# Kernel tuning notes

Hardware: AMD Instinct MI355X
Metric: run time of the kernel (lower is better)

## Reference

```python
import jax, jax.numpy as jnp
import numpy as np

EMBED_DIM = 1024
ATTN_DIM = 1024


def setup_inputs() -> dict:
    key = jax.random.key(0)
    k1, k2, k3, k4 = jax.random.split(key, 4)
    scale = 1.0 / np.sqrt(EMBED_DIM)
    return {
        "embedded": jax.random.normal(k1, (4, 2048, EMBED_DIM), dtype=jnp.float32),
        # weights stored as [in, out] (torch Linear applies x @ W.T)
        "Wk": jax.random.uniform(k2, (EMBED_DIM, ATTN_DIM), dtype=jnp.float32, minval=-scale, maxval=scale),
        "Wq": jax.random.uniform(k3, (EMBED_DIM, ATTN_DIM), dtype=jnp.float32, minval=-scale, maxval=scale),
        "Wv": jax.random.uniform(k4, (EMBED_DIM, ATTN_DIM), dtype=jnp.float32, minval=-scale, maxval=scale),
    }


def reference(embedded, Wk, Wq, Wv):
    b, t, _ = embedded.shape
    k = embedded @ Wk  # [b, t, d]
    q = embedded @ Wq
    v = embedded @ Wv
    scores = jnp.einsum("btd,bsd->bts", q, k) / jnp.sqrt(jnp.float32(k.shape[-1]))
    causal = jnp.tril(jnp.ones((t, t), dtype=bool))  # [t, t]
    scores = jnp.where(causal, scores, -jnp.inf)
    w = jax.nn.softmax(scores, axis=-1)
    o = jnp.einsum("bts,bsd->btd", w, v)
    return jnp.round(o * 10000.0) / 10000.0
```

## Files before the change

kernel.cpp:

```cpp
#include <hip/hip_runtime.h>
#include <cmath>

typedef _Float16 half8 __attribute__((ext_vector_type(8)));
typedef _Float16 half4 __attribute__((ext_vector_type(4)));
typedef float floatx4 __attribute__((ext_vector_type(4)));

__device__ __forceinline__ void load_lds16(const void* g, void* l) {
  __builtin_amdgcn_global_load_lds((const __attribute__((address_space(1))) void*)g,
                                   (__attribute__((address_space(3))) void*)l, 16, 0, 0);
}

__device__ __forceinline__ unsigned lds_addr(const void* p) {
  return (unsigned)(unsigned long long)(const __attribute__((address_space(3))) void*)p;
}

__device__ __forceinline__ half8 ds_read128(unsigned addr) {
  half8 r;
  asm volatile("ds_read_b128 %0, %1" : "=v"(r) : "v"(addr));
  return r;
}


__global__ void prep_kernel(const float* __restrict__ emb, const float* __restrict__ Wq,
                            const float* __restrict__ Wk, const float* __restrict__ Wv,
                            _Float16* __restrict__ Xp, _Float16* __restrict__ Wqp,
                            _Float16* __restrict__ Wkp, _Float16* __restrict__ Wvtp) {
  int p = blockIdx.x;
  if (p < 640) {
    __shared__ _Float16 lds[16 * 1032];
    const float* src;
    _Float16* dst;
    if (p < 512)      { src = emb + (size_t)p * 16384;        dst = Xp  + (size_t)p * 16384; }
    else if (p < 576) { src = Wq + (size_t)(p - 512) * 16384; dst = Wqp + (size_t)(p - 512) * 16384; }
    else              { src = Wk + (size_t)(p - 576) * 16384; dst = Wkp + (size_t)(p - 576) * 16384; }
    for (int it = 0; it < 16; ++it) {
      int idx = it * 256 + threadIdx.x;
      int row = idx >> 8, c4 = idx & 255;
      float4 v = ((const float4*)src)[row * 256 + c4];
      half4 h;
      h[0] = (_Float16)v.x; h[1] = (_Float16)v.y; h[2] = (_Float16)v.z; h[3] = (_Float16)v.w;
      *(half4*)(lds + row * 1032 + c4 * 4) = h;
    }
    __syncthreads();
    for (int it = 0; it < 8; ++it) {
      int c = it * 256 + threadIdx.x;
      int kb = c >> 6, k16 = (c >> 4) & 3, r = c & 15;
      half8 h = *(const half8*)(lds + r * 1032 + kb * 32 + k16 * 8);
      *(half8*)(dst + (size_t)c * 8) = h;
    }
  } else {
    __shared__ float tile[32][33];
    int q = p - 640;
    int n0 = (q & 31) * 32, k0 = (q >> 5) * 32;
    int c = threadIdx.x & 31, r8 = threadIdx.x >> 5;
    for (int pp = 0; pp < 4; ++pp) {
      int r = pp * 8 + r8;
      tile[r][c] = Wv[(size_t)(k0 + r) * 1024 + n0 + c];
    }
    __syncthreads();
    if (threadIdx.x < 128) {
      int rr = threadIdx.x & 31;
      int k16 = (threadIdx.x >> 5) & 3;
      half8 h;
      for (int kk = 0; kk < 8; ++kk) h[kk] = (_Float16)tile[k16 * 8 + kk][rr];
      int n_row = n0 + rr;
      size_t chunk = ((size_t)(n_row >> 4) * 32 + (k0 >> 5)) * 64 + (k16 << 4) + (n_row & 15);
      *(half8*)(Wvtp + chunk * 8) = h;
    }
  }
}

__device__ __forceinline__ void gemm_core_g(int lane, int wave,
                                            const _Float16* __restrict__ Ap, int kbA, int tA0,
                                            const _Float16* __restrict__ Bp, int kbB, int tB0,
                                            int kb0, int kIters, _Float16* sA, _Float16* sB,
                                            floatx4 acc[4][4]) {
  int wm = (wave >> 1) << 6, wn = (wave & 1) << 6;
  const _Float16* gA0 = Ap + ((size_t)(tA0 + 2 * wave) * kbA + kb0) * 512 + lane * 8;
  const _Float16* gA1 = Ap + ((size_t)(tA0 + 2 * wave + 1) * kbA + kb0) * 512 + lane * 8;
  const _Float16* gB0 = Bp + ((size_t)(tB0 + 2 * wave) * kbB + kb0) * 512 + lane * 8;
  const _Float16* gB1 = Bp + ((size_t)(tB0 + 2 * wave + 1) * kbB + kb0) * 512 + lane * 8;
  int ta = wm >> 4, tb = wn >> 4, lo = lane * 8;
  int wo = wave * 1024;

  load_lds16(gA0, sA + wo);
  load_lds16(gA1, sA + wo + 512);
  load_lds16(gB0, sB + wo);
  load_lds16(gB1, sB + wo + 512);
  __syncthreads();

  int cur = 0;
  for (int kt = 0; kt < kIters; ++kt) {
    if (kt + 1 < kIters) {
      size_t kb = (size_t)(kt + 1) * 512;
      int nx = (cur ^ 1) << 12;
      load_lds16(gA0 + kb, sA + nx + wo);
      load_lds16(gA1 + kb, sA + nx + wo + 512);
      load_lds16(gB0 + kb, sB + nx + wo);
      load_lds16(gB1 + kb, sB + nx + wo + 512);
    }
    const _Float16* cA = sA + (cur << 12);
    const _Float16* cB = sB + (cur << 12);
    half8 af[4], bf[4];
    for (int i = 0; i < 4; ++i) af[i] = *(const half8*)(cA + (ta + i) * 512 + lo);
    for (int j = 0; j < 4; ++j) bf[j] = *(const half8*)(cB + (tb + j) * 512 + lo);
    __builtin_amdgcn_s_setprio(1);
    for (int i = 0; i < 4; ++i)
      for (int j = 0; j < 4; ++j)
        acc[i][j] = __builtin_amdgcn_mfma_f32_16x16x32_f16(af[i], bf[j], acc[i][j], 0, 0, 0);
    __builtin_amdgcn_s_setprio(0);
    if (kt + 1 < kIters) {
      __syncthreads();
      cur ^= 1;
    }
  }
}

__device__ __forceinline__ void gemm_core(const _Float16* __restrict__ Ap, int kbA, int tA0,
                                          const _Float16* __restrict__ Bp, int kbB, int tB0,
                                          int kIters, _Float16* sA, _Float16* sB,
                                          floatx4 acc[4][4]) {
  gemm_core_g(threadIdx.x & 63, threadIdx.x >> 6, Ap, kbA, tA0, Bp, kbB, tB0, 0, kIters, sA, sB, acc);
}

__global__ void mt_kernel(const _Float16* __restrict__ Wkp, const _Float16* __restrict__ Wqp,
                          _Float16* __restrict__ Mtp) {
  __shared__ __align__(16) _Float16 sA[8192];
  __shared__ __align__(16) _Float16 sB[8192];
  floatx4 acc[4][4];
  for (int i = 0; i < 4; ++i)
    for (int j = 0; j < 4; ++j) acc[i][j] = (floatx4){0.f, 0.f, 0.f, 0.f};
  int m0 = blockIdx.y * 128, n0 = blockIdx.x * 128;
  gemm_core(Wkp, 32, m0 >> 4, Wqp, 32, n0 >> 4, 32, sA, sB, acc);
  int lane = threadIdx.x & 63, wave = threadIdx.x >> 6;
  int wm = (wave >> 1) << 6, wn = (wave & 1) << 6;
  int quad = lane >> 4, cl = lane & 15;
  for (int i = 0; i < 4; ++i)
    for (int j = 0; j < 4; ++j)
      for (int rr = 0; rr < 4; ++rr) {
        int row = m0 + wm + i * 16 + quad * 4 + rr;
        int col = n0 + wn + j * 16 + cl;
        size_t chunk = ((size_t)(row >> 4) * 32 + (col >> 5)) * 64 + (((col >> 3) & 3) << 4) + (row & 15);
        Mtp[chunk * 8 + (col & 7)] = (_Float16)acc[i][j][rr];
      }
}

#define NT_PROJ 16

__global__ __launch_bounds__(512, 2) void proj256_kernel(
    const _Float16* __restrict__ Ap, const _Float16* __restrict__ Bp,
    _Float16* __restrict__ XMp, _Float16* __restrict__ Vtp) {
  __shared__ __align__(16) _Float16 sh[65536];
  int tid = threadIdx.x;
  int lane = tid & 63, w = tid >> 6;
  int wr = w >> 2, wc = w & 3;
  int orig = blockIdx.x;
  int tile = (orig & 7) * 32 + (orig >> 3);
  int mtile = tile >> 3, ntile = tile & 7;
  int tA0 = mtile * 16, tB0 = ntile * 16;

  const _Float16* gB[4];
  int ldsB[4];
  for (int i = 0; i < 4; ++i) {
    int cb = w * 4 + i, pc = cb >> 1, kb = cb & 1;
    gB[i] = Bp + ((size_t)(tB0 + pc) * 32 + kb) * 512 + lane * 8;
    ldsB[i] = 16384 + cb * 512;
  }
  const _Float16* gA[4];
  int ldsA[4];
  {
    int kbw = w & 1, pihi = (w >> 2) * 8, pilo = (w >> 1) & 1;
    for (int q = 0; q < 4; ++q) {
      int p = 2 * q + pilo + pihi;
      gA[q] = Ap + ((size_t)(tA0 + p) * 32 + kbw) * 512 + lane * 8;
      ldsA[q] = (p * 2 + kbw) * 512;
    }
  }

  unsigned L = lds_addr(sh);
  unsigned baseA = L + (unsigned)(wr * 16384 + lane * 16);
  unsigned baseB = L + 32768u + (unsigned)(wc * 8192 + lane * 16);

  floatx4 acc[8][4];
  for (int m = 0; m < 8; ++m)
    for (int n = 0; n < 4; ++n) acc[m][n] = (floatx4){0.f, 0.f, 0.f, 0.f};

  for (int tt = 0; tt < 2; ++tt) {
    int bo = tt << 15;
    for (int i = 0; i < 4; ++i) load_lds16(gB[i] + (size_t)tt * 1024, sh + bo + ldsB[i]);
    for (int q = 0; q < 4; ++q) load_lds16(gA[q] + (size_t)tt * 1024, sh + bo + ldsA[q]);
  }
  asm volatile("s_waitcnt vmcnt(8)" ::: "memory");
  __builtin_amdgcn_s_barrier();

  half8 bf[4][2];
#pragma unroll 2
  for (int t = 0; t < NT_PROJ; ++t) {
    int bo = (t & 1) << 15;
    unsigned bob = (unsigned)(t & 1) << 16;
    unsigned aA = baseA + bob, aB = baseB + bob;
#pragma unroll
    for (int q = 0; q < 4; ++q) {
      half8 af[2][2];
      if (q == 0) {
        for (int n = 0; n < 4; ++n)
          for (int kb = 0; kb < 2; ++kb)
            bf[n][kb] = ds_read128(aB + (unsigned)(n * 2048 + kb * 1024));
      }
      for (int mm = 0; mm < 2; ++mm)
        for (int kb = 0; kb < 2; ++kb)
          af[mm][kb] = ds_read128(aA + (unsigned)((2 * q + mm) * 2048 + kb * 1024));
      if (q == 0) {
        if (t >= 1 && t + 1 < NT_PROJ)
          load_lds16(gA[3] + (size_t)(t + 1) * 1024, sh + (bo ^ 32768) + ldsA[3]);
      } else if (q == 1) {
        if (t + 2 < NT_PROJ)
          for (int i = 0; i < 4; ++i)
            load_lds16(gB[i] + (size_t)(t + 2) * 1024, sh + bo + ldsB[i]);
      } else if (q == 2) {
        if (t + 2 < NT_PROJ) {
          load_lds16(gA[0] + (size_t)(t + 2) * 1024, sh + bo + ldsA[0]);
          load_lds16(gA[1] + (size_t)(t + 2) * 1024, sh + bo + ldsA[1]);
        }
      } else {
        if (t < NT_PROJ - 1) {
          if (t + 2 < NT_PROJ) asm volatile("s_waitcnt vmcnt(6)" ::: "memory");
          else                 asm volatile("s_waitcnt vmcnt(0)" ::: "memory");
        }
        if (t + 2 < NT_PROJ)
          load_lds16(gA[2] + (size_t)(t + 2) * 1024, sh + bo + ldsA[2]);
      }
      __builtin_amdgcn_s_barrier();
      asm volatile("s_waitcnt lgkmcnt(0)" ::: "memory");
      __builtin_amdgcn_sched_barrier(0);
      __builtin_amdgcn_s_setprio(1);
      for (int mm = 0; mm < 2; ++mm)
        for (int n = 0; n < 4; ++n)
          for (int kb = 0; kb < 2; ++kb)
            acc[2 * q + mm][n] =
                __builtin_amdgcn_mfma_f32_16x16x32_f16(af[mm][kb], bf[n][kb], acc[2 * q + mm][n], 0, 0, 0);
      __builtin_amdgcn_s_setprio(0);
      __builtin_amdgcn_sched_barrier(0);
      __builtin_amdgcn_s_barrier();
    }
  }

  int quad = lane >> 4, cl = lane & 15;
  int which = ntile >> 2;
  for (int m = 0; m < 8; ++m)
    for (int n = 0; n < 4; ++n)
      for (int rr = 0; rr < 4; ++rr) {
        int rl = wr * 128 + m * 16 + quad * 4 + rr;
        int cg = wc * 64 + n * 16 + cl;
        _Float16 val = (_Float16)acc[m][n][rr];
        int lh;
        if (which) {
          lh = (((cg >> 4) * 8 + (rl >> 5)) << 9) + (((rl >> 3) & 3) << 7) + ((cg & 15) << 3) + (rl & 7);
        } else {
          lh = (((rl >> 4) * 8 + (cg >> 5)) << 9) + (((cg >> 3) & 3) << 7) + ((rl & 15) << 3) + (cg & 7);
        }
        sh[lh] = val;
      }
  __syncthreads();
  int b = mtile >> 3;
  if (which) {
    _Float16* dst = Vtp + (size_t)b * 2097152;
    for (int p = 0; p < 16; ++p) {
      size_t GB = (((size_t)(ntile & 3) * 16 + p) * 64 + (mtile & 7) * 8) * 512;
      *(half8*)(dst + GB + tid * 8) = *(const half8*)(sh + p * 4096 + tid * 8);
    }
  } else {
    _Float16* dst = XMp + (size_t)b * 2097152;
    for (int p = 0; p < 16; ++p) {
      size_t GB = (((size_t)(mtile & 7) * 16 + p) * 32 + (ntile & 3) * 8) * 512;
      *(half8*)(dst + GB + tid * 8) = *(const half8*)(sh + p * 4096 + tid * 8);
    }
  }
}

__global__ void qke_kernel(const _Float16* __restrict__ XMp, const _Float16* __restrict__ Xp,
                           _Float16* __restrict__ E, float* __restrict__ lsum) {
  __shared__ __align__(16) _Float16 sh[16384];
  int x = blockIdx.x, b = blockIdx.y;
  int p = (x & 7) * 17 + (x >> 3);
  int ti = 0;
  while ((ti + 1) * (ti + 2) / 2 <= p) ++ti;
  int tj = p - ti * (ti + 1) / 2;
  const _Float16* Ab = XMp + (size_t)b * 2097152;
  const _Float16* Bb = Xp + (size_t)b * 2097152;
  _Float16* Eb = E + (size_t)b * 4194304;
  floatx4 acc[4][4];
  for (int i = 0; i < 4; ++i)
    for (int j = 0; j < 4; ++j) acc[i][j] = (floatx4){0.f, 0.f, 0.f, 0.f};
  gemm_core(Ab, 32, ti * 8, Bb, 32, tj * 8, 32, sh, sh + 8192, acc);
  int lane = threadIdx.x & 63, wave = threadIdx.x >> 6;
  int wm = (wave >> 1) << 6, wn = (wave & 1) << 6;
  int quad = lane >> 4, cl = lane & 15;
  float rs[4][4];
  for (int i = 0; i < 4; ++i)
    for (int rr = 0; rr < 4; ++rr) rs[i][rr] = 0.f;
  __syncthreads();
  for (int i = 0; i < 4; ++i)
    for (int j = 0; j < 4; ++j)
      for (int rr = 0; rr < 4; ++rr) {
        int rl = wm + i * 16 + quad * 4 + rr;
        int cg = wn + j * 16 + cl;
        int row = ti * 128 + rl, col = tj * 128 + cg;
        float e = 0.f;
        if (col <= row) e = __expf(acc[i][j][rr] * 0.03125f - 12.0f);
        _Float16 eh = (_Float16)e;
        rs[i][rr] += (float)eh;
        int lh = (((rl >> 4) * 4 + (cg >> 5)) << 9) + (((cg >> 3) & 3) << 7) + ((rl & 15) << 3) + (cg & 7);
        sh[lh] = eh;
      }
  __syncthreads();
  for (int pp = 0; pp < 8; ++pp) {
    size_t GB = ((size_t)(ti * 8 + pp) * 64 + tj * 4) * 512;
    *(half8*)(Eb + GB + threadIdx.x * 8) = *(const half8*)(sh + pp * 2048 + threadIdx.x * 8);
  }
  float* lb = lsum + (size_t)b * 2048;
  for (int i = 0; i < 4; ++i)
    for (int rr = 0; rr < 4; ++rr) {
      float v = rs[i][rr];
      v += __shfl_xor(v, 1, 64);
      v += __shfl_xor(v, 2, 64);
      v += __shfl_xor(v, 4, 64);
      v += __shfl_xor(v, 8, 64);
      if (cl == 0) atomicAdd(lb + ti * 128 + wm + i * 16 + quad * 4 + rr, v);
    }
}

__global__ __launch_bounds__(512, 4) void pv_kernel(
    const _Float16* __restrict__ E, const _Float16* __restrict__ Vtp,
    const float* __restrict__ lsum, float* __restrict__ out) {
  __shared__ __align__(16) _Float16 sh2[32768];
  int orig = blockIdx.x + 8 * (blockIdx.y + 16 * blockIdx.z);
  int logical = (orig & 7) * 64 + (orig >> 3);
  int n0 = (logical & 7) * 128;
  int rest = logical >> 3;
  int y = rest & 15, b = rest >> 4;
  int ti = (y & 1) ? (15 - (y >> 1)) : (y >> 1);
  const _Float16* Pb = E + (size_t)b * 4194304;
  const _Float16* Vb = Vtp + (size_t)b * 2097152;
  int tid = threadIdx.x;
  int g = tid >> 8, lane = tid & 63, wave = (tid >> 6) & 3;
  int half = (ti + 1) * 2;
  _Float16* sA = sh2 + g * 16384;
  _Float16* sB = sA + 8192;
  floatx4 acc[4][4];
  for (int i = 0; i < 4; ++i)
    for (int j = 0; j < 4; ++j) acc[i][j] = (floatx4){0.f, 0.f, 0.f, 0.f};
  gemm_core_g(lane, wave, Vb, 64, n0 >> 4, Pb, 64, ti * 8, g * half, half, sA, sB, acc);
  __syncthreads();
  floatx4* xch = (floatx4*)sh2;
  if (g == 1) {
    for (int i = 0; i < 4; ++i)
      for (int j = 0; j < 4; ++j) xch[(tid - 256) * 16 + i * 4 + j] = acc[i][j];
  }
  __syncthreads();
  if (g == 0) {
    int wm = (wave >> 1) << 6, wn = (wave & 1) << 6;
    int quad = lane >> 4, cl = lane & 15;
    const float* lb = lsum + (size_t)b * 2048;
    for (int j = 0; j < 4; ++j) {
      int t = ti * 128 + wn + j * 16 + cl;
      float inv = 1.0f / lb[t];
      float* orow = out + ((size_t)b * 2048 + t) * 1024;
      for (int i = 0; i < 4; ++i) {
        floatx4 a = acc[i][j];
        floatx4 p = xch[tid * 16 + i * 4 + j];
        int d0 = n0 + wm + i * 16 + quad * 4;
        float4 v;
        v.x = rintf((a[0] + p[0]) * inv * 10000.f) * 1e-4f;
        v.y = rintf((a[1] + p[1]) * inv * 10000.f) * 1e-4f;
        v.z = rintf((a[2] + p[2]) * inv * 10000.f) * 1e-4f;
        v.w = rintf((a[3] + p[3]) * inv * 10000.f) * 1e-4f;
        *(float4*)(orow + d0) = v;
      }
    }
  }
}

extern "C" void kernel_launch(void* const* d_in, const int* in_sizes, int n_in,
                              void* d_out, int out_size, void* d_ws, size_t ws_size,
                              hipStream_t stream) {
  const float* emb = (const float*)d_in[0];
  const float* Wk = (const float*)d_in[1];
  const float* Wq = (const float*)d_in[2];
  const float* Wv = (const float*)d_in[3];
  float* out = (float*)d_out;

  _Float16* ws = (_Float16*)d_ws;
  _Float16* Xp   = ws;
  _Float16* Wqp  = Xp + (size_t)8192 * 1024;
  _Float16* Wkp  = Wqp + (size_t)1024 * 1024;
  _Float16* Mtp  = Wkp + (size_t)1024 * 1024;
  _Float16* Wvtp = Mtp + (size_t)1024 * 1024;
  _Float16* XMp  = Wvtp + (size_t)1024 * 1024;
  _Float16* Vtp  = XMp + (size_t)8192 * 1024;
  _Float16* Ebuf = Vtp + (size_t)8192 * 1024;
  float* lsum    = (float*)(Ebuf + (size_t)16 * 1024 * 1024);

  hipMemsetAsync(lsum, 0, 4 * 2048 * sizeof(float), stream);
  prep_kernel<<<1664, 256, 0, stream>>>(emb, Wq, Wk, Wv, Xp, Wqp, Wkp, Wvtp);
  mt_kernel<<<dim3(8, 8), 256, 0, stream>>>(Wkp, Wqp, Mtp);
  proj256_kernel<<<256, 512, 0, stream>>>(Xp, Mtp, XMp, Vtp);
  qke_kernel<<<dim3(136, 4), 256, 0, stream>>>(XMp, Xp, Ebuf, lsum);
  pv_kernel<<<dim3(8, 16, 4), 512, 0, stream>>>(Ebuf, Vtp, lsum, out);
}
```

Before: 219.3 us.

## Split K dimension across two wave groups in mt and qke kernels

The mt and qke GEMM kernels now run 512 threads as two groups of four waves. Each group computes half of the K reduction into its own LDS buffers, then the second group's accumulators are exchanged through shared memory and summed by the first group, which does the epilogue. The goal is to double the waves per tile and shorten the serial K loop for these small-grid kernels (64 and 544 blocks), so latency is hidden better. In exchange it adds LDS traffic and extra barriers, and half the threads sit idle during the epilogue.

```diff
diff --git a/kernel.cpp b/kernel.cpp
--- a/kernel.cpp
+++ b/kernel.cpp
@@ -123,26 +123,40 @@
   gemm_core_g(threadIdx.x & 63, threadIdx.x >> 6, Ap, kbA, tA0, Bp, kbB, tB0, 0, kIters, sA, sB, acc);
 }
 
-__global__ void mt_kernel(const _Float16* __restrict__ Wkp, const _Float16* __restrict__ Wqp,
-                          _Float16* __restrict__ Mtp) {
-  __shared__ __align__(16) _Float16 sA[8192];
-  __shared__ __align__(16) _Float16 sB[8192];
+__global__ __launch_bounds__(512, 4) void mt_kernel(
+    const _Float16* __restrict__ Wkp, const _Float16* __restrict__ Wqp,
+    _Float16* __restrict__ Mtp) {
+  __shared__ __align__(16) _Float16 sh2[32768];
   floatx4 acc[4][4];
   for (int i = 0; i < 4; ++i)
     for (int j = 0; j < 4; ++j) acc[i][j] = (floatx4){0.f, 0.f, 0.f, 0.f};
   int m0 = blockIdx.y * 128, n0 = blockIdx.x * 128;
-  gemm_core(Wkp, 32, m0 >> 4, Wqp, 32, n0 >> 4, 32, sA, sB, acc);
-  int lane = threadIdx.x & 63, wave = threadIdx.x >> 6;
-  int wm = (wave >> 1) << 6, wn = (wave & 1) << 6;
-  int quad = lane >> 4, cl = lane & 15;
-  for (int i = 0; i < 4; ++i)
-    for (int j = 0; j < 4; ++j)
-      for (int rr = 0; rr < 4; ++rr) {
-        int row = m0 + wm + i * 16 + quad * 4 + rr;
-        int col = n0 + wn + j * 16 + cl;
-        size_t chunk = ((size_t)(row >> 4) * 32 + (col >> 5)) * 64 + (((col >> 3) & 3) << 4) + (row & 15);
-        Mtp[chunk * 8 + (col & 7)] = (_Float16)acc[i][j][rr];
-      }
+  int tid = threadIdx.x;
+  int g = tid >> 8, lane = tid & 63, wave = (tid >> 6) & 3;
+  _Float16* sA = sh2 + g * 16384;
+  _Float16* sB = sA + 8192;
+  gemm_core_g(lane, wave, Wkp, 32, m0 >> 4, Wqp, 32, n0 >> 4, g * 16, 16, sA, sB, acc);
+  __syncthreads();
+  floatx4* xch = (floatx4*)sh2;
+  if (g == 1) {
+    for (int i = 0; i < 4; ++i)
+      for (int j = 0; j < 4; ++j) xch[(tid - 256) * 16 + i * 4 + j] = acc[i][j];
+  }
+  __syncthreads();
+  if (g == 0) {
+    for (int i = 0; i < 4; ++i)
+      for (int j = 0; j < 4; ++j) acc[i][j] += xch[tid * 16 + i * 4 + j];
+    int wm = (wave >> 1) << 6, wn = (wave & 1) << 6;
+    int quad = lane >> 4, cl = lane & 15;
+    for (int i = 0; i < 4; ++i)
+      for (int j = 0; j < 4; ++j)
+        for (int rr = 0; rr < 4; ++rr) {
+          int row = m0 + wm + i * 16 + quad * 4 + rr;
+          int col = n0 + wn + j * 16 + cl;
+          size_t chunk = ((size_t)(row >> 4) * 32 + (col >> 5)) * 64 + (((col >> 3) & 3) << 4) + (row & 15);
+          Mtp[chunk * 8 + (col & 7)] = (_Float16)acc[i][j][rr];
+        }
+  }
 }
 
 #define NT_PROJ 16
@@ -278,9 +292,10 @@
   }
 }
 
-__global__ void qke_kernel(const _Float16* __restrict__ XMp, const _Float16* __restrict__ Xp,
-                           _Float16* __restrict__ E, float* __restrict__ lsum) {
-  __shared__ __align__(16) _Float16 sh[16384];
+__global__ __launch_bounds__(512, 4) void qke_kernel(
+    const _Float16* __restrict__ XMp, const _Float16* __restrict__ Xp,
+    _Float16* __restrict__ E, float* __restrict__ lsum) {
+  __shared__ __align__(16) _Float16 sh2[32768];
   int x = blockIdx.x, b = blockIdx.y;
   int p = (x & 7) * 17 + (x >> 3);
   int ti = 0;
@@ -289,45 +304,63 @@
   const _Float16* Ab = XMp + (size_t)b * 2097152;
   const _Float16* Bb = Xp + (size_t)b * 2097152;
   _Float16* Eb = E + (size_t)b * 4194304;
+  int tid = threadIdx.x;
+  int g = tid >> 8, lane = tid & 63, wave = (tid >> 6) & 3;
+  _Float16* sA = sh2 + g * 16384;
+  _Float16* sB = sA + 8192;
   floatx4 acc[4][4];
   for (int i = 0; i < 4; ++i)
     for (int j = 0; j < 4; ++j) acc[i][j] = (floatx4){0.f, 0.f, 0.f, 0.f};
-  gemm_core(Ab, 32, ti * 8, Bb, 32, tj * 8, 32, sh, sh + 8192, acc);
-  int lane = threadIdx.x & 63, wave = threadIdx.x >> 6;
+  gemm_core_g(lane, wave, Ab, 32, ti * 8, Bb, 32, tj * 8, g * 16, 16, sA, sB, acc);
+  __syncthreads();
+  floatx4* xch = (floatx4*)sh2;
+  if (g == 1) {
+    for (int i = 0; i < 4; ++i)
+      for (int j = 0; j < 4; ++j) xch[(tid - 256) * 16 + i * 4 + j] = acc[i][j];
+  }
+  __syncthreads();
+  if (g == 0) {
+    for (int i = 0; i < 4; ++i)
+      for (int j = 0; j < 4; ++j) acc[i][j] += xch[tid * 16 + i * 4 + j];
+  }
+  __syncthreads();
   int wm = (wave >> 1) << 6, wn = (wave & 1) << 6;
   int quad = lane >> 4, cl = lane & 15;
   float rs[4][4];
   for (int i = 0; i < 4; ++i)
     for (int rr = 0; rr < 4; ++rr) rs[i][rr] = 0.f;
-  __syncthreads();
-  for (int i = 0; i < 4; ++i)
-    for (int j = 0; j < 4; ++j)
+  if (g == 0) {
+    for (int i = 0; i < 4; ++i)
+      for (int j = 0; j < 4; ++j)
+        for (int rr = 0; rr < 4; ++rr) {
+          int rl = wm + i * 16 + quad * 4 + rr;
+          int cg = wn + j * 16 + cl;
+          int row = ti * 128 + rl, col = tj * 128 + cg;
+          float e = 0.f;
+          if (col <= row) e = __expf(acc[i][j][rr] * 0.03125f - 12.0f);
+          _Float16 eh = (_Float16)e;
+          rs[i][rr] += (float)eh;
+          int lh = (((rl >> 4) * 4 + (cg >> 5)) << 9) + (((cg >> 3) & 3) << 7) + ((rl & 15) << 3) + (cg & 7);
+          sh2[lh] = eh;
+        }
+  }
+  __syncthreads();
+  if (g == 0) {
+    for (int pp = 0; pp < 8; ++pp) {
+      size_t GB = ((size_t)(ti * 8 + pp) * 64 + tj * 4) * 512;
+      *(half8*)(Eb + GB + tid * 8) = *(const half8*)(sh2 + pp * 2048 + tid * 8);
+    }
+    float* lb = lsum + (size_t)b * 2048;
+    for (int i = 0; i < 4; ++i)
       for (int rr = 0; rr < 4; ++rr) {
-        int rl = wm + i * 16 + quad * 4 + rr;
-        int cg = wn + j * 16 + cl;
-        int row = ti * 128 + rl, col = tj * 128 + cg;
-        float e = 0.f;
-        if (col <= row) e = __expf(acc[i][j][rr] * 0.03125f - 12.0f);
-        _Float16 eh = (_Float16)e;
-        rs[i][rr] += (float)eh;
-        int lh = (((rl >> 4) * 4 + (cg >> 5)) << 9) + (((cg >> 3) & 3) << 7) + ((rl & 15) << 3) + (cg & 7);
-        sh[lh] = eh;
+        float v = rs[i][rr];
+        v += __shfl_xor(v, 1, 64);
+        v += __shfl_xor(v, 2, 64);
+        v += __shfl_xor(v, 4, 64);
+        v += __shfl_xor(v, 8, 64);
+        if (cl == 0) atomicAdd(lb + ti * 128 + wm + i * 16 + quad * 4 + rr, v);
       }
-  __syncthreads();
-  for (int pp = 0; pp < 8; ++pp) {
-    size_t GB = ((size_t)(ti * 8 + pp) * 64 + tj * 4) * 512;
-    *(half8*)(Eb + GB + threadIdx.x * 8) = *(const half8*)(sh + pp * 2048 + threadIdx.x * 8);
-  }
-  float* lb = lsum + (size_t)b * 2048;
-  for (int i = 0; i < 4; ++i)
-    for (int rr = 0; rr < 4; ++rr) {
-      float v = rs[i][rr];
-      v += __shfl_xor(v, 1, 64);
-      v += __shfl_xor(v, 2, 64);
-      v += __shfl_xor(v, 4, 64);
-      v += __shfl_xor(v, 8, 64);
-      if (cl == 0) atomicAdd(lb + ti * 128 + wm + i * 16 + quad * 4 + rr, v);
-    }
+  }
 }
 
 __global__ __launch_bounds__(512, 4) void pv_kernel(
@@ -403,8 +436,8 @@
 
   hipMemsetAsync(lsum, 0, 4 * 2048 * sizeof(float), stream);
   prep_kernel<<<1664, 256, 0, stream>>>(emb, Wq, Wk, Wv, Xp, Wqp, Wkp, Wvtp);
-  mt_kernel<<<dim3(8, 8), 256, 0, stream>>>(Wkp, Wqp, Mtp);
+  mt_kernel<<<dim3(8, 8), 512, 0, stream>>>(Wkp, Wqp, Mtp);
   proj256_kernel<<<256, 512, 0, stream>>>(Xp, Mtp, XMp, Vtp);
-  qke_kernel<<<dim3(136, 4), 256, 0, stream>>>(XMp, Xp, Ebuf, lsum);
+  qke_kernel<<<dim3(136, 4), 512, 0, stream>>>(XMp, Xp, Ebuf, lsum);
   pv_kernel<<<dim3(8, 16, 4), 512, 0, stream>>>(Ebuf, Vtp, lsum, out);
 }
```

Measured after the change: 224.6 us. +2.4%, slower.
